# Kernel optimization log

Measured on AMD Instinct MI355X. Metric: run time of the kernel, lower is better.

Reference implementation:

```python
import jax, jax.numpy as jnp
import numpy as np

TAU = 0.5  # init tau
EPS = 1e-8  # F.cosine_similarity eps


def setup_inputs() -> dict:
    key = jax.random.key(0)
    k1, k2 = jax.random.split(key)
    N, D, NUM_CLASSES = 4096, 1024, 128
    layer_embeds = jax.random.normal(k1, (N, D), dtype=jnp.float32)
    y_true = jax.random.randint(k2, (N,), 0, NUM_CLASSES, dtype=jnp.int64)
    return {"layer_embeds": layer_embeds, "y_true": y_true}


def reference(layer_embeds, y_true):
    N = layer_embeds.shape[0]
    # batched cosine similarity, scaled like the original: (cos + 1) * 0.5 * tau
    norms = jnp.maximum(jnp.linalg.norm(layer_embeds, axis=1), EPS)  # [N]
    cos = (layer_embeds @ layer_embeds.T) / (norms[:, None] * norms[None, :])  # [N, N]
    S = (cos + 1.0) * 0.5 * TAU

    same = y_true[:, None] == y_true[None, :]  # [N, N]
    eye = jnp.eye(N, dtype=bool)
    pos_mask = same & ~eye            # same-label pairs, j != i
    neg_mask = ~same                  # different-label pairs (diag excluded since same there)

    # column 0: first positive (in j order), else stays 0
    has_pos = pos_mask.any(axis=1)
    first_pos = jnp.argmax(pos_mask, axis=1)
    pos_val = jnp.where(has_pos, S[jnp.arange(N), first_pos], 0.0)  # [N]

    # negatives fill columns 1.. in j order: col = 1 + (#negatives with j' < j)
    negi = neg_mask.astype(jnp.int32)
    col = 1 + jnp.cumsum(negi, axis=1) - negi  # [N, N]
    W = 2 * N  # pad one dummy column for non-negative entries
    cols = jnp.where(neg_mask, col, W - 1)
    rows = jnp.broadcast_to(jnp.arange(N)[:, None], (N, N))
    loss_temp = jnp.zeros((N, W), dtype=jnp.float32)
    loss_temp = loss_temp.at[rows, cols].set(jnp.where(neg_mask, S, 0.0))
    loss_temp = loss_temp.at[:, 0].set(pos_val)
    loss_temp = loss_temp[:, : 2 * N - 1]  # [N, 2N-1], matches torch buffer

    # -log_softmax, take column 0, sum over rows, divide by N
    lse = jax.nn.logsumexp(loss_temp, axis=1)  # [N]
    loss = jnp.sum(lse - loss_temp[:, 0]) / N
    return loss
```

## Files before the change

### kernel.cpp

```cpp
#include <hip/hip_runtime.h>
#include <hip/hip_bf16.h>
#include <math.h>

#define NN 4096
#define DD 1024
#define NCLS 128
#define TAU 0.5f
#define EPSV 1e-8f

typedef __bf16 bf16;
typedef __bf16 bf16x8 __attribute__((ext_vector_type(8)));
typedef __bf16 bf16x4 __attribute__((ext_vector_type(4)));
typedef float f32x4 __attribute__((ext_vector_type(4)));

__device__ __forceinline__ void gl2lds16(const void* g, void* l) {
    __builtin_amdgcn_global_load_lds(
        (const __attribute__((address_space(1))) void*)g,
        (__attribute__((address_space(3))) void*)l,
        16, 0, 0);
}

__global__ __launch_bounds__(256) void k_prep(const float* __restrict__ X,
                                              bf16* __restrict__ Xn,
                                              float* __restrict__ rsum,
                                              const int* __restrict__ y,
                                              int* __restrict__ cnt,
                                              int* __restrict__ mn1,
                                              int* __restrict__ mn2,
                                              float* __restrict__ out) {
    int w = threadIdx.x >> 6, lane = threadIdx.x & 63;
    int row = blockIdx.x * 4 + w;
    const float* xr = X + (size_t)row * DD;
    float4 v[4];
    float ss = 0.f;
#pragma unroll
    for (int c = 0; c < 4; ++c) {
        v[c] = *(const float4*)(xr + c * 256 + lane * 4);
        ss += v[c].x * v[c].x + v[c].y * v[c].y + v[c].z * v[c].z + v[c].w * v[c].w;
    }
#pragma unroll
    for (int m = 1; m < 64; m <<= 1) ss += __shfl_xor(ss, m, 64);
    float rn = 1.f / fmaxf(sqrtf(ss), EPSV);
    if (lane == 0) rsum[row] = 0.f;
#pragma unroll
    for (int c = 0; c < 4; ++c) {
        bf16x4 o;
        o.x = (bf16)(v[c].x * rn);
        o.y = (bf16)(v[c].y * rn);
        o.z = (bf16)(v[c].z * rn);
        o.w = (bf16)(v[c].w * rn);
        *(bf16x4*)(Xn + (size_t)row * DD + c * 256 + lane * 4) = o;
    }

    if (blockIdx.x == 0) {
        __shared__ int sc[NCLS], s1[NCLS], s2[NCLS];
        int t = threadIdx.x;
        if (t < NCLS) { sc[t] = 0; s1[t] = 0x7fffffff; s2[t] = 0x7fffffff; }
        __syncthreads();
        int yv[16];
#pragma unroll
        for (int k = 0; k < 16; ++k) {
            int i = k * 256 + t;
            yv[k] = y[i];
            atomicAdd(&sc[yv[k]], 1);
            atomicMin(&s1[yv[k]], i);
        }
        __syncthreads();
#pragma unroll
        for (int k = 0; k < 16; ++k) {
            int i = k * 256 + t;
            if (s1[yv[k]] != i) atomicMin(&s2[yv[k]], i);
        }
        __syncthreads();
        if (t < NCLS) { cnt[t] = sc[t]; mn1[t] = s1[t]; mn2[t] = s2[t]; }
        if (t == 0) out[0] = 0.f;
    }
}

__global__ __launch_bounds__(256) void k_gemm(const bf16* __restrict__ Xn,
                                              const int* __restrict__ y,
                                              float* __restrict__ rowsum) {
    __shared__ __align__(16) bf16 As[128 * 64];
    __shared__ __align__(16) bf16 Bs[128 * 64];
    __shared__ int yA[128], yB[128];

    int id = blockIdx.x;
    float ff = sqrtf((float)(8 * id + 1));
    int bj = (int)((ff - 1.f) * 0.5f);
    if (bj * (bj + 1) / 2 > id) bj--;
    if ((bj + 1) * (bj + 2) / 2 <= id) bj++;
    int bi = id - bj * (bj + 1) / 2;
    const int rowA0 = bi * 128;
    const int rowB0 = bj * 128;
    const bool diag = (bi == bj);

    const int tid = threadIdx.x;
    if (tid < 128) yA[tid] = y[rowA0 + tid];
    else           yB[tid - 128] = y[rowB0 + tid - 128];

    const int lane = tid & 63;
    const int w = tid >> 6;
    const int wm = w & 1, wn = w >> 1;
    const int lr = lane >> 4, lc = lane & 15;

    f32x4 acc[4][4];
#pragma unroll
    for (int i = 0; i < 4; ++i)
#pragma unroll
        for (int j = 0; j < 4; ++j) acc[i][j] = (f32x4){0.f, 0.f, 0.f, 0.f};

    const bf16* gA[4]; const bf16* gB[4];
    bf16* lA[4]; bf16* lB[4];
#pragma unroll
    for (int q = 0; q < 4; ++q) {
        int s = q * 256 + tid;
        int row = s >> 3;
        int kg = (s & 7) ^ (row & 7);
        gA[q] = Xn + (size_t)(rowA0 + row) * DD + kg * 8;
        gB[q] = Xn + (size_t)(rowB0 + row) * DD + kg * 8;
        lA[q] = As + s * 8;
        lB[q] = Bs + s * 8;
    }

    const int sw = lc & 7;

    for (int k0 = 0; k0 < DD; k0 += 64) {
        __syncthreads();
#pragma unroll
        for (int q = 0; q < 4; ++q) {
            gl2lds16(gA[q] + k0, lA[q]);
            gl2lds16(gB[q] + k0, lB[q]);
        }
        __syncthreads();

#pragma unroll
        for (int ks = 0; ks < 2; ++ks) {
            bf16x8 af[4], bfr[4];
            int slot = (ks * 4 + lr) ^ sw;
#pragma unroll
            for (int mt = 0; mt < 4; ++mt)
                af[mt] = *(const bf16x8*)(As + (wm * 64 + mt * 16 + lc) * 64 + slot * 8);
#pragma unroll
            for (int nt = 0; nt < 4; ++nt)
                bfr[nt] = *(const bf16x8*)(Bs + (wn * 64 + nt * 16 + lc) * 64 + slot * 8);
#pragma unroll
            for (int mt = 0; mt < 4; ++mt)
#pragma unroll
                for (int nt = 0; nt < 4; ++nt)
                    acc[mt][nt] = __builtin_amdgcn_mfma_f32_16x16x32_bf16(
                        af[mt], bfr[nt], acc[mt][nt], 0, 0, 0);
        }
    }

    int ycol[4];
#pragma unroll
    for (int nt = 0; nt < 4; ++nt) ycol[nt] = yB[wn * 64 + nt * 16 + lc];
    float colacc[4] = {0.f, 0.f, 0.f, 0.f};
#pragma unroll
    for (int mt = 0; mt < 4; ++mt) {
#pragma unroll
        for (int rr = 0; rr < 4; ++rr) {
            int rloc = wm * 64 + mt * 16 + lr * 4 + rr;
            int yrow = yA[rloc];
            float s = 0.f;
#pragma unroll
            for (int nt = 0; nt < 4; ++nt) {
                float Sv = (acc[mt][nt][rr] + 1.f) * (0.5f * TAU);
                float e = (ycol[nt] != yrow) ? __expf(Sv) : 0.f;
                s += e;
                colacc[nt] += e;
            }
            s += __shfl_xor(s, 1, 16);
            s += __shfl_xor(s, 2, 16);
            s += __shfl_xor(s, 4, 16);
            s += __shfl_xor(s, 8, 16);
            if (lc == 0) atomicAdd(&rowsum[rowA0 + rloc], s);
        }
    }
    if (!diag) {
#pragma unroll
        for (int nt = 0; nt < 4; ++nt) {
            float cs = colacc[nt];
            cs += __shfl_xor(cs, 16, 64);
            cs += __shfl_xor(cs, 32, 64);
            if (lane < 16) atomicAdd(&rowsum[rowB0 + wn * 64 + nt * 16 + lane], cs);
        }
    }
}

__global__ __launch_bounds__(256) void k_tail(const bf16* __restrict__ Xn,
                                              const int* __restrict__ y,
                                              const int* __restrict__ cnt,
                                              const int* __restrict__ mn1,
                                              const int* __restrict__ mn2,
                                              const float* __restrict__ rowsum,
                                              float* __restrict__ out) {
    int w = threadIdx.x >> 6, lane = threadIdx.x & 63;
    int i = blockIdx.x * 4 + w;
    int c = y[i];
    int cc = cnt[c];
    float pv = 0.f;
    if (cc >= 2) {
        int fp = (mn1[c] == i) ? mn2[c] : mn1[c];
        const bf16* xi = Xn + (size_t)i * DD;
        const bf16* xf = Xn + (size_t)fp * DD;
        float dot = 0.f;
#pragma unroll
        for (int q = 0; q < 2; ++q) {
            bf16x8 a = *(const bf16x8*)(xi + q * 512 + lane * 8);
            bf16x8 b = *(const bf16x8*)(xf + q * 512 + lane * 8);
#pragma unroll
            for (int e = 0; e < 8; ++e) dot += (float)a[e] * (float)b[e];
        }
#pragma unroll
        for (int m = 1; m < 64; m <<= 1) dot += __shfl_xor(dot, m, 64);
        pv = (dot + 1.f) * (0.5f * TAU);
    }
    float contrib = logf(rowsum[i] + __expf(pv) + (float)(NN - 2 + cc)) - pv;
    __shared__ float wsum[4];
    if (lane == 0) wsum[w] = contrib;
    __syncthreads();
    if (threadIdx.x == 0)
        atomicAdd(out, (wsum[0] + wsum[1] + wsum[2] + wsum[3]) * (1.f / (float)NN));
}

extern "C" void kernel_launch(void* const* d_in, const int* in_sizes, int n_in,
                              void* d_out, int out_size, void* d_ws, size_t ws_size,
                              hipStream_t stream) {
    const float* X = (const float*)d_in[0];
    const int* y = (const int*)d_in[1];
    float* out = (float*)d_out;

    char* ws = (char*)d_ws;
    bf16* Xn    = (bf16*)ws;
    float* rsum = (float*)(ws + 8 * 1024 * 1024);
    int* cnt    = (int*)(ws + 8 * 1024 * 1024 + 16 * 1024);
    int* mn1    = (int*)(ws + 8 * 1024 * 1024 + 16 * 1024 + 512);
    int* mn2    = (int*)(ws + 8 * 1024 * 1024 + 16 * 1024 + 1024);

    k_prep<<<dim3(NN / 4), 256, 0, stream>>>(X, Xn, rsum, y, cnt, mn1, mn2, out);
    k_gemm<<<dim3(528), 256, 0, stream>>>(Xn, y, rsum);
    k_tail<<<dim3(NN / 4), 256, 0, stream>>>(Xn, y, cnt, mn1, mn2, rsum, out);
}
```

Baseline: 127.5 us.

## Split GEMM tiles into 128x64 halves with two-wave blocks and K=32 steps

Each triangular 128x128 tile is now handled by two blocks, one per 64-column half. Each block uses 128 threads (two waves, each computing 64x64), a K-step of 32 instead of 64, and a matching 4-slot LDS swizzle. This doubles the grid to 1056 blocks and shrinks LDS per block. The aim is better occupancy and load balance across the CUs. The cost is that A-tile loads are duplicated across the half-blocks and there are twice as many sync barriers per K.

```diff
diff --git a/kernel.cpp b/kernel.cpp
--- a/kernel.cpp
+++ b/kernel.cpp
@@ -77,30 +77,30 @@
     }
 }
 
-__global__ __launch_bounds__(256) void k_gemm(const bf16* __restrict__ Xn,
+__global__ __launch_bounds__(128) void k_gemm(const bf16* __restrict__ Xn,
                                               const int* __restrict__ y,
                                               float* __restrict__ rowsum) {
-    __shared__ __align__(16) bf16 As[128 * 64];
-    __shared__ __align__(16) bf16 Bs[128 * 64];
-    __shared__ int yA[128], yB[128];
-
-    int id = blockIdx.x;
-    float ff = sqrtf((float)(8 * id + 1));
+    __shared__ __align__(16) bf16 As[128 * 32];
+    __shared__ __align__(16) bf16 Bs[64 * 32];
+    __shared__ int yA[128], yB[64];
+
+    int t = blockIdx.x >> 1;
+    int h = blockIdx.x & 1;
+    float ff = sqrtf((float)(8 * t + 1));
     int bj = (int)((ff - 1.f) * 0.5f);
-    if (bj * (bj + 1) / 2 > id) bj--;
-    if ((bj + 1) * (bj + 2) / 2 <= id) bj++;
-    int bi = id - bj * (bj + 1) / 2;
+    if (bj * (bj + 1) / 2 > t) bj--;
+    if ((bj + 1) * (bj + 2) / 2 <= t) bj++;
+    int bi = t - bj * (bj + 1) / 2;
     const int rowA0 = bi * 128;
-    const int rowB0 = bj * 128;
+    const int colB0 = bj * 128 + h * 64;
     const bool diag = (bi == bj);
 
     const int tid = threadIdx.x;
-    if (tid < 128) yA[tid] = y[rowA0 + tid];
-    else           yB[tid - 128] = y[rowB0 + tid - 128];
+    yA[tid] = y[rowA0 + tid];
+    if (tid < 64) yB[tid] = y[colB0 + tid];
 
     const int lane = tid & 63;
     const int w = tid >> 6;
-    const int wm = w & 1, wn = w >> 1;
     const int lr = lane >> 4, lc = lane & 15;
 
     f32x4 acc[4][4];
@@ -109,58 +109,60 @@
 #pragma unroll
         for (int j = 0; j < 4; ++j) acc[i][j] = (f32x4){0.f, 0.f, 0.f, 0.f};
 
-    const bf16* gA[4]; const bf16* gB[4];
-    bf16* lA[4]; bf16* lB[4];
+    const bf16* gA[4]; bf16* lA[4];
 #pragma unroll
     for (int q = 0; q < 4; ++q) {
-        int s = q * 256 + tid;
-        int row = s >> 3;
-        int kg = (s & 7) ^ (row & 7);
+        int s = q * 128 + tid;
+        int row = s >> 2, g = s & 3;
+        int kg = g ^ ((row >> 1) & 3);
         gA[q] = Xn + (size_t)(rowA0 + row) * DD + kg * 8;
-        gB[q] = Xn + (size_t)(rowB0 + row) * DD + kg * 8;
         lA[q] = As + s * 8;
+    }
+    const bf16* gB[2]; bf16* lB[2];
+#pragma unroll
+    for (int q = 0; q < 2; ++q) {
+        int s = q * 128 + tid;
+        int row = s >> 2, g = s & 3;
+        int kg = g ^ ((row >> 1) & 3);
+        gB[q] = Xn + (size_t)(colB0 + row) * DD + kg * 8;
         lB[q] = Bs + s * 8;
     }
 
-    const int sw = lc & 7;
-
-    for (int k0 = 0; k0 < DD; k0 += 64) {
-        __syncthreads();
-#pragma unroll
-        for (int q = 0; q < 4; ++q) {
-            gl2lds16(gA[q] + k0, lA[q]);
-            gl2lds16(gB[q] + k0, lB[q]);
-        }
-        __syncthreads();
-
-#pragma unroll
-        for (int ks = 0; ks < 2; ++ks) {
-            bf16x8 af[4], bfr[4];
-            int slot = (ks * 4 + lr) ^ sw;
-#pragma unroll
-            for (int mt = 0; mt < 4; ++mt)
-                af[mt] = *(const bf16x8*)(As + (wm * 64 + mt * 16 + lc) * 64 + slot * 8);
+    const int sw = (lc >> 1) & 3;
+    const int slot = lr ^ sw;
+
+    for (int k0 = 0; k0 < DD; k0 += 32) {
+        __syncthreads();
+#pragma unroll
+        for (int q = 0; q < 4; ++q) gl2lds16(gA[q] + k0, lA[q]);
+#pragma unroll
+        for (int q = 0; q < 2; ++q) gl2lds16(gB[q] + k0, lB[q]);
+        __syncthreads();
+
+        bf16x8 af[4], bfr[4];
+#pragma unroll
+        for (int mt = 0; mt < 4; ++mt)
+            af[mt] = *(const bf16x8*)(As + (w * 64 + mt * 16 + lc) * 32 + slot * 8);
+#pragma unroll
+        for (int nt = 0; nt < 4; ++nt)
+            bfr[nt] = *(const bf16x8*)(Bs + (nt * 16 + lc) * 32 + slot * 8);
+#pragma unroll
+        for (int mt = 0; mt < 4; ++mt)
 #pragma unroll
             for (int nt = 0; nt < 4; ++nt)
-                bfr[nt] = *(const bf16x8*)(Bs + (wn * 64 + nt * 16 + lc) * 64 + slot * 8);
-#pragma unroll
-            for (int mt = 0; mt < 4; ++mt)
-#pragma unroll
-                for (int nt = 0; nt < 4; ++nt)
-                    acc[mt][nt] = __builtin_amdgcn_mfma_f32_16x16x32_bf16(
-                        af[mt], bfr[nt], acc[mt][nt], 0, 0, 0);
-        }
+                acc[mt][nt] = __builtin_amdgcn_mfma_f32_16x16x32_bf16(
+                    af[mt], bfr[nt], acc[mt][nt], 0, 0, 0);
     }
 
     int ycol[4];
 #pragma unroll
-    for (int nt = 0; nt < 4; ++nt) ycol[nt] = yB[wn * 64 + nt * 16 + lc];
+    for (int nt = 0; nt < 4; ++nt) ycol[nt] = yB[nt * 16 + lc];
     float colacc[4] = {0.f, 0.f, 0.f, 0.f};
 #pragma unroll
     for (int mt = 0; mt < 4; ++mt) {
 #pragma unroll
         for (int rr = 0; rr < 4; ++rr) {
-            int rloc = wm * 64 + mt * 16 + lr * 4 + rr;
+            int rloc = w * 64 + mt * 16 + lr * 4 + rr;
             int yrow = yA[rloc];
             float s = 0.f;
 #pragma unroll
@@ -183,7 +185,7 @@
             float cs = colacc[nt];
             cs += __shfl_xor(cs, 16, 64);
             cs += __shfl_xor(cs, 32, 64);
-            if (lane < 16) atomicAdd(&rowsum[rowB0 + wn * 64 + nt * 16 + lane], cs);
+            if (lane < 16) atomicAdd(&rowsum[colB0 + nt * 16 + lane], cs);
         }
     }
 }
@@ -239,6 +241,6 @@
     int* mn2    = (int*)(ws + 8 * 1024 * 1024 + 16 * 1024 + 1024);
 
     k_prep<<<dim3(NN / 4), 256, 0, stream>>>(X, Xn, rsum, y, cnt, mn1, mn2, out);
-    k_gemm<<<dim3(528), 256, 0, stream>>>(Xn, y, rsum);
+    k_gemm<<<dim3(1056), 128, 0, stream>>>(Xn, y, rsum);
     k_tail<<<dim3(NN / 4), 256, 0, stream>>>(Xn, y, cnt, mn1, mn2, rsum, out);
 }
```

Result: no change. 126.1 us (-1.1%).

## Quantize normalized embeddings to FP8 and run Gram GEMM with FP8 MFMA

Applied to the files above, without the earlier changes.

The prep kernel now also writes a scaled FP8 (e4m3) copy of the normalized embeddings, with a x16 scale to use more of the FP8 range. The Gram GEMM loads these FP8 tiles with a new LDS swizzle and uses the 16x16x32 fp8 MFMA, halving operand bytes and raising MFMA throughput. The epilogue divides out the 256 scale factor. The tail still uses bf16 for the positive-pair dot. The cost is lower precision in the similarity sums, which may affect how closely the loss matches the reference.

```diff
diff --git a/kernel.cpp b/kernel.cpp
--- a/kernel.cpp
+++ b/kernel.cpp
@@ -12,6 +12,7 @@
 typedef __bf16 bf16x8 __attribute__((ext_vector_type(8)));
 typedef __bf16 bf16x4 __attribute__((ext_vector_type(4)));
 typedef float f32x4 __attribute__((ext_vector_type(4)));
+typedef unsigned char u8;
 
 __device__ __forceinline__ void gl2lds16(const void* g, void* l) {
     __builtin_amdgcn_global_load_lds(
@@ -20,8 +21,15 @@
         16, 0, 0);
 }
 
+__device__ __forceinline__ unsigned pk8(float4 v, float s) {
+    int lo = __builtin_amdgcn_cvt_pk_fp8_f32(v.x * s, v.y * s, 0, false);
+    int r  = __builtin_amdgcn_cvt_pk_fp8_f32(v.z * s, v.w * s, lo, true);
+    return (unsigned)r;
+}
+
 __global__ __launch_bounds__(256) void k_prep(const float* __restrict__ X,
                                               bf16* __restrict__ Xn,
+                                              u8* __restrict__ Xq,
                                               float* __restrict__ rsum,
                                               const int* __restrict__ y,
                                               int* __restrict__ cnt,
@@ -50,6 +58,7 @@
         o.z = (bf16)(v[c].z * rn);
         o.w = (bf16)(v[c].w * rn);
         *(bf16x4*)(Xn + (size_t)row * DD + c * 256 + lane * 4) = o;
+        *(unsigned*)(Xq + (size_t)row * DD + c * 256 + lane * 4) = pk8(v[c], rn * 16.f);
     }
 
     if (blockIdx.x == 0) {
@@ -77,11 +86,11 @@
     }
 }
 
-__global__ __launch_bounds__(256) void k_gemm(const bf16* __restrict__ Xn,
+__global__ __launch_bounds__(256) void k_gemm(const u8* __restrict__ Xq,
                                               const int* __restrict__ y,
                                               float* __restrict__ rowsum) {
-    __shared__ __align__(16) bf16 As[128 * 64];
-    __shared__ __align__(16) bf16 Bs[128 * 64];
+    __shared__ __align__(16) u8 As[128 * 64];
+    __shared__ __align__(16) u8 Bs[128 * 64];
     __shared__ int yA[128], yB[128];
 
     int id = blockIdx.x;
@@ -109,25 +118,24 @@
 #pragma unroll
         for (int j = 0; j < 4; ++j) acc[i][j] = (f32x4){0.f, 0.f, 0.f, 0.f};
 
-    const bf16* gA[4]; const bf16* gB[4];
-    bf16* lA[4]; bf16* lB[4];
-#pragma unroll
-    for (int q = 0; q < 4; ++q) {
-        int s = q * 256 + tid;
-        int row = s >> 3;
-        int kg = (s & 7) ^ (row & 7);
-        gA[q] = Xn + (size_t)(rowA0 + row) * DD + kg * 8;
-        gB[q] = Xn + (size_t)(rowB0 + row) * DD + kg * 8;
-        lA[q] = As + s * 8;
-        lB[q] = Bs + s * 8;
-    }
-
-    const int sw = lc & 7;
+    const u8* gA[2]; const u8* gB[2]; u8* lA[2]; u8* lB[2];
+#pragma unroll
+    for (int q = 0; q < 2; ++q) {
+        int m = q * 256 + tid;
+        int row = m >> 2;
+        int a = (m & 3) ^ ((row >> 1) & 3);
+        gA[q] = Xq + (size_t)(rowA0 + row) * DD + a * 16;
+        gB[q] = Xq + (size_t)(rowB0 + row) * DD + a * 16;
+        lA[q] = As + m * 16;
+        lB[q] = Bs + m * 16;
+    }
+
+    const int psw = 2 * ((lc >> 1) & 3);
 
     for (int k0 = 0; k0 < DD; k0 += 64) {
         __syncthreads();
 #pragma unroll
-        for (int q = 0; q < 4; ++q) {
+        for (int q = 0; q < 2; ++q) {
             gl2lds16(gA[q] + k0, lA[q]);
             gl2lds16(gB[q] + k0, lB[q]);
         }
@@ -135,19 +143,19 @@
 
 #pragma unroll
         for (int ks = 0; ks < 2; ++ks) {
-            bf16x8 af[4], bfr[4];
-            int slot = (ks * 4 + lr) ^ sw;
+            int pos = (ks * 4 + lr) ^ psw;
+            long af[4], bfr[4];
 #pragma unroll
             for (int mt = 0; mt < 4; ++mt)
-                af[mt] = *(const bf16x8*)(As + (wm * 64 + mt * 16 + lc) * 64 + slot * 8);
+                af[mt] = *(const long*)(As + (wm * 64 + mt * 16 + lc) * 64 + pos * 8);
 #pragma unroll
             for (int nt = 0; nt < 4; ++nt)
-                bfr[nt] = *(const bf16x8*)(Bs + (wn * 64 + nt * 16 + lc) * 64 + slot * 8);
+                bfr[nt] = *(const long*)(Bs + (wn * 64 + nt * 16 + lc) * 64 + pos * 8);
 #pragma unroll
             for (int mt = 0; mt < 4; ++mt)
 #pragma unroll
                 for (int nt = 0; nt < 4; ++nt)
-                    acc[mt][nt] = __builtin_amdgcn_mfma_f32_16x16x32_bf16(
+                    acc[mt][nt] = __builtin_amdgcn_mfma_f32_16x16x32_fp8_fp8(
                         af[mt], bfr[nt], acc[mt][nt], 0, 0, 0);
         }
     }
@@ -165,7 +173,7 @@
             float s = 0.f;
 #pragma unroll
             for (int nt = 0; nt < 4; ++nt) {
-                float Sv = (acc[mt][nt][rr] + 1.f) * (0.5f * TAU);
+                float Sv = acc[mt][nt][rr] * (0.25f / 256.f) + 0.25f;
                 float e = (ycol[nt] != yrow) ? __expf(Sv) : 0.f;
                 s += e;
                 colacc[nt] += e;
@@ -233,12 +241,13 @@
 
     char* ws = (char*)d_ws;
     bf16* Xn    = (bf16*)ws;
-    float* rsum = (float*)(ws + 8 * 1024 * 1024);
-    int* cnt    = (int*)(ws + 8 * 1024 * 1024 + 16 * 1024);
-    int* mn1    = (int*)(ws + 8 * 1024 * 1024 + 16 * 1024 + 512);
-    int* mn2    = (int*)(ws + 8 * 1024 * 1024 + 16 * 1024 + 1024);
-
-    k_prep<<<dim3(NN / 4), 256, 0, stream>>>(X, Xn, rsum, y, cnt, mn1, mn2, out);
-    k_gemm<<<dim3(528), 256, 0, stream>>>(Xn, y, rsum);
+    u8*   Xq    = (u8*)(ws + 8 * 1024 * 1024);
+    float* rsum = (float*)(ws + 12 * 1024 * 1024);
+    int* cnt    = (int*)(ws + 12 * 1024 * 1024 + 16 * 1024);
+    int* mn1    = (int*)(ws + 12 * 1024 * 1024 + 16 * 1024 + 512);
+    int* mn2    = (int*)(ws + 12 * 1024 * 1024 + 16 * 1024 + 1024);
+
+    k_prep<<<dim3(NN / 4), 256, 0, stream>>>(X, Xn, Xq, rsum, y, cnt, mn1, mn2, out);
+    k_gemm<<<dim3(528), 256, 0, stream>>>(Xq, y, rsum);
     k_tail<<<dim3(NN / 4), 256, 0, stream>>>(Xn, y, cnt, mn1, mn2, rsum, out);
 }
```

Result: faster. 122.3 us (-4.1%).
